# Kernel optimization log

Measured on AMD Instinct MI355X. Metric: run time of the kernel, lower is better.

## Reference

```python
import jax, jax.numpy as jnp
import numpy as np

B, S, H = 2, 2048, 2048
DK = DV = 128
HK, HV = 16, 32
G = HV // HK          # num_v_groups = 2
K = 4                 # conv kernel size
EPS = 1e-6
FQKVZ = 2 * HK * DK + 2 * HV * DV   # 12288
FBA = 2 * HV                        # 64
C = 2 * HK * DK + HV * DV           # conv channels = 8192


def setup_inputs() -> dict:
    key = jax.random.key(0)
    ks = jax.random.split(key, 10)
    f32 = jnp.float32
    return {
        "x": jax.random.normal(ks[0], (B, S, H), f32),
        "w_qkvz": jax.random.normal(ks[1], (H, FQKVZ), f32) * 0.02,
        "w_ba": jax.random.normal(ks[2], (H, FBA), f32) * 0.02,
        "conv_w": jax.random.normal(ks[3], (C, K), f32) * 0.1,
        "conv_b": jax.random.normal(ks[4], (C,), f32) * 0.02,
        "a_log": jax.random.normal(ks[5], (HV,), f32) * 0.5,
        "dt_bias": jax.random.normal(ks[6], (HV,), f32) * 0.5,
        "norm_w": jnp.ones((DV,), f32),
        "w_o": jax.random.normal(ks[7], (HV * DV, H), f32) * 0.02,
    }


def _l2norm(t):
    return t * jax.lax.rsqrt(jnp.sum(t * t, axis=-1, keepdims=True) + EPS)


def reference(x, w_qkvz, w_ba, conv_w, conv_b, a_log, dt_bias, norm_w, w_o):
    # fused input projections
    qkvz = x @ w_qkvz                                   # [B,S,FQKVZ]
    ba = x @ w_ba                                       # [B,S,FBA]

    # split_fused_inputs: per k-head layout [q(DK), k(DK), v(G*DV), z(G*DV)]
    qkvz = qkvz.reshape(B, S, HK, 2 * DK + 2 * G * DV)
    q = qkvz[..., :DK]                                  # [B,S,HK,DK]
    k = qkvz[..., DK:2 * DK]
    v = qkvz[..., 2 * DK:2 * DK + G * DV].reshape(B, S, HV, DV)
    z = qkvz[..., 2 * DK + G * DV:].reshape(B, S, HV, DV)
    ba = ba.reshape(B, S, HK, 2 * G)
    b = ba[..., :G].reshape(B, S, HV)
    a = ba[..., G:].reshape(B, S, HV)

    # causal depthwise conv1d + silu over concat(q,k,v) channels
    mixed = jnp.concatenate(
        [q.reshape(B, S, HK * DK), k.reshape(B, S, HK * DK), v.reshape(B, S, HV * DV)],
        axis=-1).transpose(0, 2, 1)                     # [B,C,S]
    mixed = jnp.pad(mixed, ((0, 0), (0, 0), (K - 1, 0)))
    mixed = jax.lax.conv_general_dilated(
        mixed, conv_w[:, None, :], (1,), 'VALID',
        dimension_numbers=('NCH', 'OIH', 'NCH'), feature_group_count=C)
    mixed = jax.nn.silu(mixed + conv_b[None, :, None]).transpose(0, 2, 1)  # [B,S,C]

    kd = HK * DK
    q = mixed[..., :kd].reshape(B, S, HK, DK)
    k = mixed[..., kd:2 * kd].reshape(B, S, HK, DK)
    v = mixed[..., 2 * kd:].reshape(B, S, HV, DV)

    # gating params
    g = -jnp.exp(a_log) * jax.nn.softplus(a + dt_bias)  # [B,S,HV]
    beta = jax.nn.sigmoid(b)                            # [B,S,HV]

    # GQA expand + qk l2-norm (kernel applies l2norm inside)
    q = jnp.repeat(q, G, axis=2)                        # [B,S,HV,DK]
    k = jnp.repeat(k, G, axis=2)
    q = _l2norm(q) * (DK ** -0.5)
    k = _l2norm(k)

    # gated delta-rule recurrence: S_t = exp(g_t) S_{t-1} + k_t (beta_t (v_t - k_t^T S))
    def step(Sm, inp):
        q_t, k_t, v_t, g_t, b_t = inp                   # [B,HV,*]
        Sm = Sm * jnp.exp(g_t)[..., None, None]
        kS = jnp.einsum('bhk,bhkv->bhv', k_t, Sm)
        dv = b_t[..., None] * (v_t - kS)
        Sm = Sm + k_t[..., None] * dv[:, :, None, :]
        o_t = jnp.einsum('bhk,bhkv->bhv', q_t, Sm)
        return Sm, o_t

    S0 = jnp.zeros((B, HV, DK, DV), q.dtype)
    seq = (jnp.moveaxis(q, 1, 0), jnp.moveaxis(k, 1, 0), jnp.moveaxis(v, 1, 0),
           jnp.moveaxis(g, 1, 0), jnp.moveaxis(beta, 1, 0))
    _, o = jax.lax.scan(step, S0, seq)                  # o: [S,B,HV,DV]
    o = jnp.moveaxis(o, 0, 1)                           # [B,S,HV,DV]

    # gated RMSNorm (Mamba-style: gate before norm)
    y = o * jax.nn.silu(z)
    var = jnp.mean(y * y, axis=-1, keepdims=True)
    y = y * jax.lax.rsqrt(var + EPS) * norm_w

    return y.reshape(B, S, HV * DV) @ w_o               # [B,S,H]
```

## Files before the change

kernel.cpp:

```cpp
#include <hip/hip_runtime.h>

typedef _Float16 f16;
typedef _Float16 f16x2 __attribute__((ext_vector_type(2)));
typedef _Float16 f16x4 __attribute__((ext_vector_type(4)));
typedef _Float16 f16x8 __attribute__((ext_vector_type(8)));
typedef float f32x4 __attribute__((ext_vector_type(4)));

#define QSCALE 0.08838834764831845f

#define RAW_BARRIER() do { \
    asm volatile("s_waitcnt lgkmcnt(0)" ::: "memory"); \
    __builtin_amdgcn_s_barrier(); \
    __builtin_amdgcn_sched_barrier(0); \
} while (0)

__global__ __launch_bounds__(256) void cvt16_kernel(const float* __restrict__ in,
                                                    f16* __restrict__ out, int n4) {
    int i = blockIdx.x * 256 + threadIdx.x;
    if (i >= n4) return;
    f32x4 v = ((const f32x4*)in)[i];
    f16x4 h;
    h[0] = (f16)v[0]; h[1] = (f16)v[1]; h[2] = (f16)v[2]; h[3] = (f16)v[3];
    ((f16x4*)out)[i] = h;
}

__global__ __launch_bounds__(256) void transpose16_kernel(const float* __restrict__ in,
                                                          f16* __restrict__ out, int R, int C) {
    __shared__ f16 tile[64][66];
    int c0 = blockIdx.x * 64, r0 = blockIdx.y * 64;
    int tid = threadIdx.x;
#pragma unroll
    for (int i = 0; i < 16; ++i) {
        int idx = i * 256 + tid;
        int r = idx >> 6, c = idx & 63;
        tile[r][c] = (f16)in[(long)(r0 + r) * C + (c0 + c)];
    }
    __syncthreads();
#pragma unroll
    for (int i = 0; i < 16; ++i) {
        int idx = i * 256 + tid;
        int orow = idx >> 6, oc = idx & 63;
        out[(long)(c0 + orow) * R + (r0 + oc)] = tile[oc][orow];
    }
}

template <int NJ, int F16OUT>
__global__ __launch_bounds__(512, 1) void gemm256_kernel(const f16* __restrict__ A,
                                                         const f16* __restrict__ Bt,
                                                         void* __restrict__ Cout,
                                                         int M, int N, int Kd) {
    constexpr int BN = 64 * NJ;
    constexpr int BNW = 16 * NJ;
    __shared__ f16 sA[2][256 * 64];
    __shared__ f16 sB[2][BN * 64];
    const int tid = threadIdx.x;
    const int lane = tid & 63, wv = tid >> 6;
    const int wm = wv >> 2, wn = wv & 3;
    const int m0 = blockIdx.y * 256, n0 = blockIdx.x * BN;
    const int lrow = lane & 15, lk = lane >> 4;
    const int nK = Kd >> 6;

    f32x4 acc[8][NJ] = {};
    f32x4 ra[4], rb[NJ];

    auto issue = [&](int k0) {
#pragma unroll
        for (int j = 0; j < 4; ++j) {
            int P = (tid + j * 512) * 16;
            int row = P >> 7;
            int koff = (P & 127) >> 1;
            ra[j] = *(const f32x4*)(A + (long)(m0 + row) * Kd + k0 + koff);
        }
#pragma unroll
        for (int j = 0; j < NJ; ++j) {
            int P = (tid + j * 512) * 16;
            int row = P >> 7;
            int koff = (P & 127) >> 1;
            rb[j] = *(const f32x4*)(Bt + (long)(n0 + row) * Kd + k0 + koff);
        }
    };
    auto commit = [&](int buf) {
#pragma unroll
        for (int j = 0; j < 4; ++j) {
            int P = (tid + j * 512) * 16;
            int row = P >> 7;
            int sw = P ^ ((row & 7) << 4);
            *(f32x4*)((char*)&sA[buf][0] + sw) = ra[j];
        }
#pragma unroll
        for (int j = 0; j < NJ; ++j) {
            int P = (tid + j * 512) * 16;
            int row = P >> 7;
            int sw = P ^ ((row & 7) << 4);
            *(f32x4*)((char*)&sB[buf][0] + sw) = rb[j];
        }
    };

    issue(0);
    commit(0);
    if (nK > 1) issue(64);
    RAW_BARRIER();

    int cur = 0;
    for (int t = 0; t < nK; ++t) {
        if (t + 1 < nK) commit(cur ^ 1);
        if (t + 2 < nK) issue((t + 2) * 64);
        const char* bA = (const char*)&sA[cur][0];
        const char* bB = (const char*)&sB[cur][0];
        __builtin_amdgcn_s_setprio(1);
#pragma unroll
        for (int kk = 0; kk < 2; ++kk) {
            f16x8 bf[NJ];
#pragma unroll
            for (int j = 0; j < NJ; ++j) {
                int brow = wn * BNW + j * 16 + lrow;
                int bbyte = brow * 128 + kk * 64 + lk * 16;
                bf[j] = *(const f16x8*)(bB + (bbyte ^ ((brow & 7) << 4)));
            }
#pragma unroll
            for (int i = 0; i < 8; ++i) {
                int arow = wm * 128 + i * 16 + lrow;
                int abyte = arow * 128 + kk * 64 + lk * 16;
                f16x8 af = *(const f16x8*)(bA + (abyte ^ ((arow & 7) << 4)));
#pragma unroll
                for (int j = 0; j < NJ; ++j)
                    acc[i][j] = __builtin_amdgcn_mfma_f32_16x16x32_f16(af, bf[j], acc[i][j], 0, 0, 0);
            }
        }
        __builtin_amdgcn_s_setprio(0);
        RAW_BARRIER();
        cur ^= 1;
    }

#pragma unroll
    for (int i = 0; i < 8; ++i) {
        int gm_base = m0 + wm * 128 + i * 16 + lk * 4;
#pragma unroll
        for (int j = 0; j < NJ; ++j) {
            int gn = n0 + wn * BNW + j * 16 + lrow;
#pragma unroll
            for (int r = 0; r < 4; ++r) {
                long idx = (long)(gm_base + r) * N + gn;
                if (F16OUT) ((f16*)Cout)[idx] = (f16)acc[i][j][r];
                else        ((float*)Cout)[idx] = acc[i][j][r];
            }
        }
    }
}

__global__ __launch_bounds__(256) void ba_gemm_kernel(const float* __restrict__ x,
                                                      const float* __restrict__ w,
                                                      const float* __restrict__ a_log,
                                                      const float* __restrict__ dt_bias,
                                                      float* __restrict__ gout,
                                                      float* __restrict__ bt) {
    __shared__ float xs[16][256];
    int tid = threadIdx.x;
    int t0 = blockIdx.x * 16;
    int o = tid & 63, tg = tid >> 6;
    float acc[4] = {0.f, 0.f, 0.f, 0.f};
    for (int kc = 0; kc < 2048; kc += 256) {
        __syncthreads();
#pragma unroll
        for (int i = 0; i < 16; ++i) {
            int idx = i * 256 + tid;
            int tok = idx >> 8, k = idx & 255;
            xs[tok][k] = x[(long)(t0 + tok) * 2048 + kc + k];
        }
        __syncthreads();
        for (int k = 0; k < 256; ++k) {
            float wv = w[(long)(kc + k) * 64 + o];
#pragma unroll
            for (int j = 0; j < 4; ++j) acc[j] += xs[tg * 4 + j][k] * wv;
        }
    }
    int hv = ((o >> 2) << 1) | (o & 1);
    bool isB = (o & 2) == 0;
    float al = expf(a_log[hv]);
    float db = dt_bias[hv];
#pragma unroll
    for (int j = 0; j < 4; ++j) {
        int tok = t0 + tg * 4 + j;
        int b = tok >> 11, s = tok & 2047;
        long oidx = ((long)b * 32 + hv) * 2048 + s;
        if (isB) {
            bt[oidx] = 1.f / (1.f + expf(-acc[j]));
        } else {
            float xx = acc[j] + db;
            float sp = (xx > 20.f) ? xx : log1pf(expf(xx));
            gout[oidx] = -al * sp;
        }
    }
}

__global__ __launch_bounds__(256) void conv_kernel(const f16* __restrict__ qkvz,
                                                   const float* __restrict__ cw,
                                                   const float* __restrict__ cb,
                                                   f16* __restrict__ qh,
                                                   f16* __restrict__ kh,
                                                   f16* __restrict__ vh,
                                                   f16* __restrict__ khT) {
    __shared__ float Lin[35 * 128];
    __shared__ float Lout[32 * 128];
    __shared__ float Lsc[32];
    int g = blockIdx.x;
    int s0 = blockIdx.y * 32;
    int b = blockIdx.z;
    int tid = threadIdx.x;
    int colbase, chbase;
    f16* outp;
    bool donorm;
    bool isk = false;
    int hk = 0;
    float nmul;
    if (g < 16) {
        colbase = g * 768; chbase = g * 128;
        outp = qh + (((long)b * 16 + g) * 2048 + s0) * 128;
        donorm = true; nmul = QSCALE;
    } else if (g < 32) {
        hk = g - 16;
        colbase = hk * 768 + 128; chbase = 2048 + hk * 128;
        outp = kh + (((long)b * 16 + hk) * 2048 + s0) * 128;
        donorm = true; nmul = 1.f; isk = true;
    } else {
        int hv = g - 32;
        colbase = (hv >> 1) * 768 + 256 + (hv & 1) * 128; chbase = 4096 + hv * 128;
        outp = vh + (((long)b * 32 + hv) * 2048 + s0) * 128;
        donorm = false; nmul = 1.f;
    }
    for (int ci = tid; ci < 35 * 16; ci += 256) {
        int sr = ci >> 4, cc = (ci & 15) * 8;
        int s = s0 + sr - 3;
        f32x4 lo = {}, hi = {};
        if (s >= 0) {
            f16x8 v = *(const f16x8*)(qkvz + ((long)b * 2048 + s) * 12288 + colbase + cc);
#pragma unroll
            for (int e = 0; e < 4; ++e) { lo[e] = (float)v[e]; hi[e] = (float)v[4 + e]; }
        }
        *(f32x4*)&Lin[sr * 128 + cc] = lo;
        *(f32x4*)&Lin[sr * 128 + cc + 4] = hi;
    }
    __syncthreads();
    int c = tid & 127, sg = tid >> 7;
    float w0 = cw[(chbase + c) * 4 + 0];
    float w1 = cw[(chbase + c) * 4 + 1];
    float w2 = cw[(chbase + c) * 4 + 2];
    float w3 = cw[(chbase + c) * 4 + 3];
    float bias = cb[chbase + c];
#pragma unroll
    for (int j = 0; j < 16; ++j) {
        int sl = sg * 16 + j;
        float v = w0 * Lin[sl * 128 + c] + w1 * Lin[(sl + 1) * 128 + c] +
                  w2 * Lin[(sl + 2) * 128 + c] + w3 * Lin[(sl + 3) * 128 + c] + bias;
        v = v / (1.f + expf(-v));
        Lout[sl * 128 + c] = v;
    }
    __syncthreads();
    if (donorm) {
        int token = tid >> 3, part = tid & 7;
        float ss = 0.f;
#pragma unroll
        for (int i = 0; i < 16; ++i) {
            float v = Lout[token * 128 + part * 16 + i];
            ss += v * v;
        }
        ss += __shfl_xor(ss, 1); ss += __shfl_xor(ss, 2); ss += __shfl_xor(ss, 4);
        if (part == 0) Lsc[token] = rsqrtf(ss + 1e-6f) * nmul;
        __syncthreads();
#pragma unroll
        for (int j = 0; j < 16; ++j) {
            int sl = sg * 16 + j;
            outp[(long)sl * 128 + c] = (f16)(Lout[sl * 128 + c] * Lsc[sl]);
        }
        if (isk) {
            int dk = tid >> 1, sh = tid & 1;
            f16x8 v0, v1;
#pragma unroll
            for (int i = 0; i < 8; ++i) {
                v0[i] = (f16)(Lout[(sh * 16 + i) * 128 + dk] * Lsc[sh * 16 + i]);
                v1[i] = (f16)(Lout[(sh * 16 + 8 + i) * 128 + dk] * Lsc[sh * 16 + 8 + i]);
            }
            f16* kt = khT + ((long)(b * 16 + hk) * 128 + dk) * 2048 + s0 + sh * 16;
            *(f16x8*)kt = v0;
            *(f16x8*)(kt + 8) = v1;
        }
    } else {
#pragma unroll
        for (int j = 0; j < 16; ++j) {
            int sl = sg * 16 + j;
            outp[(long)sl * 128 + c] = (f16)Lout[sl * 128 + c];
        }
    }
}

__global__ __launch_bounds__(64) void chunk_pre_kernel(const f16* __restrict__ qh,
                                                       const f16* __restrict__ kh,
                                                       const f16* __restrict__ vh,
                                                       const float* __restrict__ gb,
                                                       const float* __restrict__ bt,
                                                       f16* __restrict__ Wg,
                                                       f16* __restrict__ T2ng,
                                                       f16* __restrict__ d0g,
                                                       float* __restrict__ pvg) {
    __shared__ f16 VTl[128 * 32];
    __shared__ float KKl[32 * 32];
    __shared__ float RL[32 * 32];
    __shared__ float Tf[32 * 33];
    __shared__ f16 Tl[32 * 64];
    __shared__ float cuml[32], bl[32], pl[32];

    int bid = blockIdx.x;
    int chunk = bid & 63;
    int hv = (bid >> 6) & 31;
    int b = bid >> 11;
    int bh = b * 16 + (hv >> 1);
    int l = threadIdx.x;
    int h = l >> 4, c = l & 15;
    long chid = bid;

    const f16* kbase = kh + ((long)bh * 2048 + chunk * 32) * 128;
    const f16* qbase = qh + ((long)bh * 2048 + chunk * 32) * 128;
    const f16* vbase = vh + (((long)b * 32 + hv) * 2048 + chunk * 32) * 128;
    const float* gp = gb + ((long)b * 32 + hv) * 2048 + chunk * 32;
    const float* bp = bt + ((long)b * 32 + hv) * 2048 + chunk * 32;

    f16x8 fk[2][4], fq[2][4];
#pragma unroll
    for (int ti = 0; ti < 2; ++ti)
#pragma unroll
        for (int kk = 0; kk < 4; ++kk) {
            fk[ti][kk] = *(const f16x8*)(kbase + (c + 16 * ti) * 128 + kk * 32 + h * 8);
            fq[ti][kk] = *(const f16x8*)(qbase + (c + 16 * ti) * 128 + kk * 32 + h * 8);
        }

    float gv = (l < 32) ? gp[l] : 0.f;
#pragma unroll
    for (int d = 1; d < 32; d <<= 1) {
        float t2 = __shfl_up(gv, d);
        if (l >= d) gv += t2;
    }
    if (l < 32) { cuml[l] = gv; bl[l] = bp[l]; pl[l] = expf(gv); }
    __syncthreads();

#pragma unroll
    for (int it = 0; it < 8; ++it) {
        int idx = (l + it * 64) * 8;
        int row = idx >> 7, col = idx & 127;
        f16x8 v = *(const f16x8*)(vbase + (long)row * 128 + col);
        float be = bl[row];
#pragma unroll
        for (int e = 0; e < 8; ++e) {
            int dv = col + e;
            int byte = (dv * 64 + row * 2) ^ ((dv & 3) << 4);
            *(f16*)((char*)VTl + byte) = (f16)((float)v[e] * be);
        }
    }
#pragma unroll
    for (int it = 0; it < 16; ++it) {
        int e = l * 16 + it;
        int i = e >> 5, j = e & 31;
        RL[e] = (j <= i) ? expf(cuml[i] - cuml[j]) : 0.f;
    }
    __syncthreads();

    {
        f32x4 acc[2][2] = {};
#pragma unroll
        for (int kk = 0; kk < 4; ++kk) {
            acc[0][0] = __builtin_amdgcn_mfma_f32_16x16x32_f16(fk[0][kk], fk[0][kk], acc[0][0], 0, 0, 0);
            acc[0][1] = __builtin_amdgcn_mfma_f32_16x16x32_f16(fk[0][kk], fk[1][kk], acc[0][1], 0, 0, 0);
            acc[1][0] = __builtin_amdgcn_mfma_f32_16x16x32_f16(fk[1][kk], fk[0][kk], acc[1][0], 0, 0, 0);
            acc[1][1] = __builtin_amdgcn_mfma_f32_16x16x32_f16(fk[1][kk], fk[1][kk], acc[1][1], 0, 0, 0);
        }
#pragma unroll
        for (int ti = 0; ti < 2; ++ti)
#pragma unroll
            for (int tj = 0; tj < 2; ++tj)
#pragma unroll
                for (int r = 0; r < 4; ++r)
                    KKl[(h * 4 + r + 16 * ti) * 32 + c + 16 * tj] = acc[ti][tj][r];
    }
    {
        f32x4 acc[2][2] = {};
#pragma unroll
        for (int kk = 0; kk < 4; ++kk) {
            acc[0][0] = __builtin_amdgcn_mfma_f32_16x16x32_f16(fq[0][kk], fk[0][kk], acc[0][0], 0, 0, 0);
            acc[0][1] = __builtin_amdgcn_mfma_f32_16x16x32_f16(fq[0][kk], fk[1][kk], acc[0][1], 0, 0, 0);
            acc[1][0] = __builtin_amdgcn_mfma_f32_16x16x32_f16(fq[1][kk], fk[0][kk], acc[1][0], 0, 0, 0);
            acc[1][1] = __builtin_amdgcn_mfma_f32_16x16x32_f16(fq[1][kk], fk[1][kk], acc[1][1], 0, 0, 0);
        }
        __syncthreads();
#pragma unroll
        for (int ti = 0; ti < 2; ++ti)
#pragma unroll
            for (int tj = 0; tj < 2; ++tj)
#pragma unroll
                for (int r = 0; r < 4; ++r) {
                    int i = h * 4 + r + 16 * ti, j = c + 16 * tj;
                    Wg[chid * 1024 + i * 32 + j] = (f16)(acc[ti][tj][r] * RL[i * 32 + j]);
                }
    }

    if (l < 32) {
        int j = l;
        for (int i = 0; i < 32; ++i) {
            float s = (i == j) ? 1.f : 0.f;
            float bi = bl[i];
            for (int ll = j; ll < i; ++ll)
                s -= bi * KKl[i * 32 + ll] * RL[i * 32 + ll] * Tf[ll * 33 + j];
            Tf[i * 33 + j] = s;
        }
        float bpj = bl[j] * pl[j];
        for (int i = 0; i < 32; ++i) {
            float tv = (i >= j) ? Tf[i * 33 + j] : 0.f;
            int byte = (i * 128 + j * 2) ^ ((i & 3) << 4);
            *(f16*)((char*)Tl + byte) = (f16)tv;
            T2ng[chid * 1024 + i * 32 + j] = (f16)(-tv * bpj);
        }
        pvg[chid * 64 + j] = pl[j];
        pvg[chid * 64 + 32 + j] = expf(cuml[31] - cuml[j]);
    }
    __syncthreads();

    {
        f16x8 fT[2];
#pragma unroll
        for (int ti = 0; ti < 2; ++ti) {
            int row = c + 16 * ti;
            fT[ti] = *(const f16x8*)((const char*)Tl + ((row * 128 + h * 16) ^ ((row & 3) << 4)));
        }
#pragma unroll
        for (int nj = 0; nj < 8; ++nj) {
            int dv = c + 16 * nj;
            f16x8 fv = *(const f16x8*)((const char*)VTl + ((dv * 64 + h * 16) ^ ((dv & 3) << 4)));
            f32x4 a0 = {}, a1 = {};
            a0 = __builtin_amdgcn_mfma_f32_16x16x32_f16(fT[0], fv, a0, 0, 0, 0);
            a1 = __builtin_amdgcn_mfma_f32_16x16x32_f16(fT[1], fv, a1, 0, 0, 0);
            f16x4 s0, s1;
#pragma unroll
            for (int r = 0; r < 4; ++r) { s0[r] = (f16)a0[r]; s1[r] = (f16)a1[r]; }
            *(f16x4*)(d0g + chid * 4096 + (long)dv * 32 + 4 * h) = s0;
            *(f16x4*)(d0g + chid * 4096 + (long)dv * 32 + 16 + 4 * h) = s1;
        }
    }
}

struct CR {
    f16x8 fk[2][4], fq[2][4], fkt[8], fT[2], fW[2];
    f16x4 fd0[2];
    f32x4 pva, pvb, kwa, kwb;
    float pc;
};

__global__ __launch_bounds__(64, 1) void scan_kernel(const f16* __restrict__ qh,
                                                     const f16* __restrict__ kh,
                                                     const f16* __restrict__ khT,
                                                     const f16* __restrict__ Wg,
                                                     const f16* __restrict__ T2ng,
                                                     const f16* __restrict__ d0g,
                                                     const float* __restrict__ pvg,
                                                     f16* __restrict__ ob) {
    __shared__ f16 Sl[2][16 * 128];
    __shared__ f16 AKl[16 * 32];
    __shared__ f16 Dl[16 * 32];

    int pbid = blockIdx.x;
    int bid = (pbid & 7) * 64 + (pbid >> 3);
    int vs = bid & 7;
    int hv = (bid >> 3) & 31;
    int b = bid >> 8;
    int bh32 = b * 32 + hv;
    int bh = b * 16 + (hv >> 1);
    int l = threadIdx.x, h = l >> 4, c = l & 15;

    const f16* kb = kh + (long)bh * 2048 * 128;
    const f16* qb = qh + (long)bh * 2048 * 128;
    const f16* ktb = khT + (long)bh * 128 * 2048;

    f16x8 z = {};
#pragma unroll
    for (int it = 0; it < 4; ++it) *(f16x8*)((char*)Sl[0] + (l + it * 64) * 16) = z;

    int cur = 0;

    auto loadC = [&](CR& R, int ch) {
        long chid = (long)bh32 * 64 + ch;
#pragma unroll
        for (int ti = 0; ti < 2; ++ti) {
            long row = (long)ch * 32 + c + 16 * ti;
#pragma unroll
            for (int kk = 0; kk < 4; ++kk) {
                R.fk[ti][kk] = *(const f16x8*)(kb + row * 128 + kk * 32 + h * 8);
                R.fq[ti][kk] = *(const f16x8*)(qb + row * 128 + kk * 32 + h * 8);
            }
            R.fT[ti] = *(const f16x8*)(T2ng + chid * 1024 + (c + 16 * ti) * 32 + h * 8);
            R.fW[ti] = *(const f16x8*)(Wg + chid * 1024 + (c + 16 * ti) * 32 + h * 8);
        }
#pragma unroll
        for (int ti = 0; ti < 8; ++ti)
            R.fkt[ti] = *(const f16x8*)(ktb + (long)(c + 16 * ti) * 2048 + ch * 32 + h * 8);
#pragma unroll
        for (int ti = 0; ti < 2; ++ti)
            R.fd0[ti] = *(const f16x4*)(d0g + chid * 4096 +
                                        (long)(vs * 16 + c) * 32 + 16 * ti + 4 * h);
        R.pva = *(const f32x4*)(pvg + chid * 64 + 4 * h);
        R.pvb = *(const f32x4*)(pvg + chid * 64 + 16 + 4 * h);
        R.pc = pvg[chid * 64 + 31];
        R.kwa = *(const f32x4*)(pvg + chid * 64 + 32 + h * 8);
        R.kwb = *(const f32x4*)(pvg + chid * 64 + 36 + h * 8);
    };

    auto computeC = [&](const CR& R, int ch) {
        const int dv = c;
        f16x8 fS[4];
#pragma unroll
        for (int kk = 0; kk < 4; ++kk)
            fS[kk] = *(const f16x8*)((char*)Sl[cur] +
                                     (dv * 256 + ((kk * 64 + h * 16) ^ ((dv & 7) << 4))));
        f32x4 AK[2] = {}, AQ[2] = {};
#pragma unroll
        for (int ti = 0; ti < 2; ++ti)
#pragma unroll
            for (int kk = 0; kk < 4; ++kk) {
                AK[ti] = __builtin_amdgcn_mfma_f32_16x16x32_f16(R.fk[ti][kk], fS[kk], AK[ti], 0, 0, 0);
                AQ[ti] = __builtin_amdgcn_mfma_f32_16x16x32_f16(R.fq[ti][kk], fS[kk], AQ[ti], 0, 0, 0);
            }
#pragma unroll
        for (int ti = 0; ti < 2; ++ti) {
            f16x4 t;
#pragma unroll
            for (int r = 0; r < 4; ++r) t[r] = (f16)AK[ti][r];
            *(f16x4*)((char*)AKl + ((dv * 64 + 32 * ti + 8 * h) ^ ((dv & 3) << 4))) = t;
        }
        f32x4 Dv[2];
#pragma unroll
        for (int ti = 0; ti < 2; ++ti)
#pragma unroll
            for (int r = 0; r < 4; ++r) Dv[ti][r] = (float)R.fd0[ti][r];
        {
            f16x8 fak = *(const f16x8*)((char*)AKl + ((dv * 64 + h * 16) ^ ((dv & 3) << 4)));
#pragma unroll
            for (int ti = 0; ti < 2; ++ti)
                Dv[ti] = __builtin_amdgcn_mfma_f32_16x16x32_f16(R.fT[ti], fak, Dv[ti], 0, 0, 0);
        }
#pragma unroll
        for (int ti = 0; ti < 2; ++ti) {
            f16x4 t;
#pragma unroll
            for (int r = 0; r < 4; ++r) t[r] = (f16)Dv[ti][r];
            *(f16x4*)((char*)Dl + ((dv * 64 + 32 * ti + 8 * h) ^ ((dv & 3) << 4))) = t;
        }
        f16x8 fdl = *(const f16x8*)((char*)Dl + ((dv * 64 + h * 16) ^ ((dv & 3) << 4)));
        f32x4 Ov[2];
#pragma unroll
        for (int ti = 0; ti < 2; ++ti)
#pragma unroll
            for (int r = 0; r < 4; ++r)
                Ov[ti][r] = AQ[ti][r] * (ti ? R.pvb[r] : R.pva[r]);
#pragma unroll
        for (int ti = 0; ti < 2; ++ti)
            Ov[ti] = __builtin_amdgcn_mfma_f32_16x16x32_f16(R.fW[ti], fdl, Ov[ti], 0, 0, 0);
#pragma unroll
        for (int ti = 0; ti < 2; ++ti)
#pragma unroll
            for (int r = 0; r < 4; ++r) {
                long tok = (long)b * 2048 + ch * 32 + 16 * ti + 4 * h + r;
                ob[tok * 4096 + hv * 128 + vs * 16 + c] = (f16)Ov[ti][r];
            }
#pragma unroll
        for (int ti = 0; ti < 8; ++ti) {
            f16x8 fa;
#pragma unroll
            for (int e = 0; e < 8; ++e)
                fa[e] = (f16)((float)R.fkt[ti][e] * (e < 4 ? R.kwa[e] : R.kwb[e - 4]));
            int sbyte = (dv * 256 + (32 * ti + 8 * h)) ^ ((dv & 7) << 4);
            f16x4 sold = *(const f16x4*)((char*)Sl[cur] + sbyte);
            f32x4 acc;
#pragma unroll
            for (int r = 0; r < 4; ++r) acc[r] = R.pc * (float)sold[r];
            acc = __builtin_amdgcn_mfma_f32_16x16x32_f16(fa, fdl, acc, 0, 0, 0);
            f16x4 snew;
#pragma unroll
            for (int r = 0; r < 4; ++r) snew[r] = (f16)acc[r];
            *(f16x4*)((char*)Sl[cur ^ 1] + sbyte) = snew;
        }
        cur ^= 1;
        RAW_BARRIER();
    };

    CR A, B;
    loadC(A, 0);
    RAW_BARRIER();
    for (int ch = 0; ch < 64; ch += 2) {
        loadC(B, ch + 1);
        computeC(A, ch);
        loadC(A, ch + 2 < 64 ? ch + 2 : 63);
        computeC(B, ch + 1);
    }
}

__global__ __launch_bounds__(256) void gate_kernel(const f16* __restrict__ o,
                                                   const f16* __restrict__ qkvz,
                                                   const float* __restrict__ norm_w,
                                                   f16* __restrict__ y) {
    int token = blockIdx.x;
    int tid = threadIdx.x;
    int hv = tid >> 3, part = tid & 7;
    int dv0 = part * 16;
    const f16* orow = o + ((long)token * 32 + hv) * 128 + dv0;
    long zcol = (long)(hv >> 1) * 768 + 512 + (hv & 1) * 128 + dv0;
    const f16* zrow = qkvz + (long)token * 12288 + zcol;
    f16x8 ov0 = *(const f16x8*)orow, ov1 = *(const f16x8*)(orow + 8);
    f16x8 zv0 = *(const f16x8*)zrow, zv1 = *(const f16x8*)(zrow + 8);
    float yv[16];
    float ss = 0.f;
#pragma unroll
    for (int i = 0; i < 16; ++i) {
        float ovf = (float)(i < 8 ? ov0[i] : ov1[i - 8]);
        float zvf = (float)(i < 8 ? zv0[i] : zv1[i - 8]);
        float gt = zvf / (1.f + expf(-zvf));
        float v = ovf * gt;
        yv[i] = v;
        ss += v * v;
    }
    ss += __shfl_xor(ss, 1); ss += __shfl_xor(ss, 2); ss += __shfl_xor(ss, 4);
    float scale = rsqrtf(ss * (1.f / 128.f) + 1e-6f);
    f16* yrow = y + (long)token * 4096 + hv * 128 + dv0;
    f16x8 y0, y1;
#pragma unroll
    for (int i = 0; i < 8; ++i) {
        y0[i] = (f16)(yv[i] * scale * norm_w[dv0 + i]);
        y1[i] = (f16)(yv[8 + i] * scale * norm_w[dv0 + 8 + i]);
    }
    *(f16x8*)yrow = y0;
    *(f16x8*)(yrow + 8) = y1;
}

extern "C" void kernel_launch(void* const* d_in, const int* in_sizes, int n_in,
                              void* d_out, int out_size, void* d_ws, size_t ws_size,
                              hipStream_t stream) {
    const float* x       = (const float*)d_in[0];
    const float* w_qkvz  = (const float*)d_in[1];
    const float* w_ba    = (const float*)d_in[2];
    const float* conv_w  = (const float*)d_in[3];
    const float* conv_b  = (const float*)d_in[4];
    const float* a_log   = (const float*)d_in[5];
    const float* dt_bias = (const float*)d_in[6];
    const float* norm_w  = (const float*)d_in[7];
    const float* w_o     = (const float*)d_in[8];
    float* out = (float*)d_out;

    char* ws = (char*)d_ws;
    const size_t MB = 1024 * 1024;
    f16*   qkvz16 = (f16*)ws;
    f16*   x16    = (f16*)(ws + 96 * MB);
    f16*   WT     = (f16*)(ws + 112 * MB);
    f16*   d0g    = (f16*)(ws + 96 * MB);
    f16*   Wg     = (f16*)(ws + 128 * MB);
    f16*   T2ng   = (f16*)(ws + 136 * MB);
    f16*   khT    = (f16*)(ws + 144 * MB);
    f16*   WTo    = (f16*)(ws + 160 * MB);
    f16*   qh     = (f16*)(ws + 176 * MB);
    f16*   kh     = (f16*)(ws + 192 * MB);
    f16*   vh     = (f16*)(ws + 208 * MB);
    f16*   ob     = (f16*)(ws + 208 * MB);
    f16*   y16    = (f16*)(ws + 176 * MB);
    float* gbuf   = (float*)(ws + 240 * MB);
    float* btb    = (float*)(ws + 240 * MB + 512 * 1024);
    float* pvg    = (float*)(ws + 241 * MB);

    cvt16_kernel<<<8192, 256, 0, stream>>>(x, x16, 4096 * 2048 / 4);
    transpose16_kernel<<<dim3(12288 / 64, 2048 / 64), 256, 0, stream>>>(w_qkvz, WT, 2048, 12288);
    transpose16_kernel<<<dim3(2048 / 64, 4096 / 64), 256, 0, stream>>>(w_o, WTo, 4096, 2048);

    gemm256_kernel<4, 1><<<dim3(12288 / 256, 4096 / 256), 512, 0, stream>>>(x16, WT, qkvz16, 4096, 12288, 2048);
    ba_gemm_kernel<<<256, 256, 0, stream>>>(x, w_ba, a_log, dt_bias, gbuf, btb);

    conv_kernel<<<dim3(64, 64, 2), 256, 0, stream>>>(qkvz16, conv_w, conv_b, qh, kh, vh, khT);
    chunk_pre_kernel<<<4096, 64, 0, stream>>>(qh, kh, vh, gbuf, btb, Wg, T2ng, d0g, pvg);
    scan_kernel<<<512, 64, 0, stream>>>(qh, kh, khT, Wg, T2ng, d0g, pvg, ob);

    gate_kernel<<<4096, 256, 0, stream>>>(ob, qkvz16, norm_w, y16);

    gemm256_kernel<2, 0><<<dim3(2048 / 128, 4096 / 256), 512, 0, stream>>>(y16, WTo, out, 4096, 2048, 4096);
}
```

Before: 748.0 us.

## Move GEMM prefetch after MFMA loop and parallelize ba projection over tokens

In the main GEMM, the LDS commit and next global prefetch now run after the MFMA block instead of before it, which changes how global loads overlap with compute. The ba projection kernel now has each block handle 4 tokens with 1024 blocks instead of 16 tokens with 256 blocks. Each block stages whole rows of x in LDS with vectorized loads and each thread accumulates one output. This spreads the small ba GEMM over more CUs, at the cost of reading w_ba four times as often. Moving the prefetch may shorten or lengthen the exposed global-load latency in the GEMM pipeline.

```diff
diff --git a/kernel.cpp b/kernel.cpp
--- a/kernel.cpp
+++ b/kernel.cpp
@@ -103,8 +103,6 @@
 
     int cur = 0;
     for (int t = 0; t < nK; ++t) {
-        if (t + 1 < nK) commit(cur ^ 1);
-        if (t + 2 < nK) issue((t + 2) * 64);
         const char* bA = (const char*)&sA[cur][0];
         const char* bB = (const char*)&sB[cur][0];
         __builtin_amdgcn_s_setprio(1);
@@ -128,6 +126,8 @@
             }
         }
         __builtin_amdgcn_s_setprio(0);
+        if (t + 1 < nK) commit(cur ^ 1);
+        if (t + 2 < nK) issue((t + 2) * 64);
         RAW_BARRIER();
         cur ^= 1;
     }
@@ -154,42 +154,31 @@
                                                       const float* __restrict__ dt_bias,
                                                       float* __restrict__ gout,
                                                       float* __restrict__ bt) {
-    __shared__ float xs[16][256];
+    __shared__ float xs[4][2048];
     int tid = threadIdx.x;
-    int t0 = blockIdx.x * 16;
+    int t0 = blockIdx.x * 4;
     int o = tid & 63, tg = tid >> 6;
-    float acc[4] = {0.f, 0.f, 0.f, 0.f};
-    for (int kc = 0; kc < 2048; kc += 256) {
-        __syncthreads();
-#pragma unroll
-        for (int i = 0; i < 16; ++i) {
-            int idx = i * 256 + tid;
-            int tok = idx >> 8, k = idx & 255;
-            xs[tok][k] = x[(long)(t0 + tok) * 2048 + kc + k];
-        }
-        __syncthreads();
-        for (int k = 0; k < 256; ++k) {
-            float wv = w[(long)(kc + k) * 64 + o];
-#pragma unroll
-            for (int j = 0; j < 4; ++j) acc[j] += xs[tg * 4 + j][k] * wv;
-        }
-    }
+    for (int i = tid; i < 4 * 512; i += 256) {
+        int tok = i >> 9, kq = i & 511;
+        ((f32x4*)&xs[tok][0])[kq] = ((const f32x4*)(x + (long)(t0 + tok) * 2048))[kq];
+    }
+    __syncthreads();
+    const float* xr = &xs[tg][0];
+    float acc = 0.f;
+    for (int k = 0; k < 2048; ++k)
+        acc = fmaf(xr[k], w[(long)k * 64 + o], acc);
+
     int hv = ((o >> 2) << 1) | (o & 1);
     bool isB = (o & 2) == 0;
-    float al = expf(a_log[hv]);
-    float db = dt_bias[hv];
-#pragma unroll
-    for (int j = 0; j < 4; ++j) {
-        int tok = t0 + tg * 4 + j;
-        int b = tok >> 11, s = tok & 2047;
-        long oidx = ((long)b * 32 + hv) * 2048 + s;
-        if (isB) {
-            bt[oidx] = 1.f / (1.f + expf(-acc[j]));
-        } else {
-            float xx = acc[j] + db;
-            float sp = (xx > 20.f) ? xx : log1pf(expf(xx));
-            gout[oidx] = -al * sp;
-        }
+    int tok = t0 + tg;
+    int b = tok >> 11, s = tok & 2047;
+    long oidx = ((long)b * 32 + hv) * 2048 + s;
+    if (isB) {
+        bt[oidx] = 1.f / (1.f + expf(-acc));
+    } else {
+        float xx = acc + dt_bias[hv];
+        float sp = (xx > 20.f) ? xx : log1pf(expf(xx));
+        gout[oidx] = -expf(a_log[hv]) * sp;
     }
 }
 
@@ -674,7 +663,7 @@
     transpose16_kernel<<<dim3(2048 / 64, 4096 / 64), 256, 0, stream>>>(w_o, WTo, 4096, 2048);
 
     gemm256_kernel<4, 1><<<dim3(12288 / 256, 4096 / 256), 512, 0, stream>>>(x16, WT, qkvz16, 4096, 12288, 2048);
-    ba_gemm_kernel<<<256, 256, 0, stream>>>(x, w_ba, a_log, dt_bias, gbuf, btb);
+    ba_gemm_kernel<<<1024, 256, 0, stream>>>(x, w_ba, a_log, dt_bias, gbuf, btb);
 
     conv_kernel<<<dim3(64, 64, 2), 256, 0, stream>>>(qkvz16, conv_w, conv_b, qh, kh, vh, khT);
     chunk_pre_kernel<<<4096, 64, 0, stream>>>(qh, kh, vh, gbuf, btb, Wg, T2ng, d0g, pvg);
```

Result: faster. 694.4 us (-7.2%).
